# Optimization experiments

Hardware: AMD Instinct MI355X
Metric: run time of the kernel (lower is better)

Reference implementation:

```python
import jax, jax.numpy as jnp
import numpy as np

B, S = 16384, 2048
EPS = 1e-8


def _autocorr(x, lag):
    # Pearson correlation between x[:, :-lag] and x[:, lag:] (ddof cancels).
    a = x[:, :-lag]
    b = x[:, lag:]
    am = a.mean(axis=1, keepdims=True)
    bm = b.mean(axis=1, keepdims=True)
    cov = ((a - am) * (b - bm)).mean(axis=1)
    return cov / (a.std(axis=1) * b.std(axis=1))


def _stat_features(x):
    S_len = x.shape[1]
    mean = x.mean(axis=1)
    xc = x - mean[:, None]
    m2 = (xc ** 2).mean(axis=1)
    m3 = (xc ** 3).mean(axis=1)
    m4 = (xc ** 4).mean(axis=1)
    std = jnp.sqrt(m2)
    min_v = x.min(axis=1)
    max_v = x.max(axis=1)
    q = jnp.percentile(x, jnp.array([25.0, 50.0, 75.0]), axis=1)  # [3, B]
    p25, median, p75 = q[0], q[1], q[2]
    diff = jnp.diff(x, axis=1)
    std_diff = diff.std(axis=1)
    trend = std_diff / (std + EPS)
    ac1 = _autocorr(x, 1)
    ac7 = _autocorr(x, 7)
    ac24 = _autocorr(x, 24)
    cv = std / (jnp.abs(mean) + EPS)
    iqr = p75 - p25
    seasonal = x[:, ::24].var(axis=1) / (m2 + EPS)
    skew = m3 / (m2 ** 1.5)          # scipy.stats.skew, bias=True
    kurt = m4 / (m2 ** 2) - 3.0      # scipy.stats.kurtosis, Fisher, bias=True
    length = jnp.full_like(mean, float(S_len))
    sum_abs_diff = jnp.abs(diff).sum(axis=1)
    mean_abs_diff = jnp.abs(diff).mean(axis=1)
    feats = jnp.stack([mean, std, min_v, max_v, median, trend, ac1, ac7, ac24,
                       cv, iqr, seasonal, skew, kurt, length,
                       sum_abs_diff, mean_abs_diff, std_diff, p25, p75], axis=1)
    return jnp.where(jnp.isfinite(feats), feats, 0.0)


def setup_inputs() -> dict:
    key = jax.random.key(0)
    k0, k1, k2, k3, k4 = jax.random.split(key, 5)
    x = jax.random.normal(k0, (B, S), dtype=jnp.float32)
    W1 = jax.random.normal(k1, (64, 20), dtype=jnp.float32) * 0.1
    b1 = jnp.zeros((64,), dtype=jnp.float32)
    W2 = jax.random.normal(k3, (128, 64), dtype=jnp.float32) * 0.1
    b2 = jnp.zeros((128,), dtype=jnp.float32)
    return {"x": x, "W1": W1, "b1": b1, "W2": W2, "b2": b2}


def reference(x, W1, b1, W2, b2):
    feats = _stat_features(x)                      # [B, 20]
    h = jax.nn.relu(feats @ W1.T + b1)             # [B, 64] (dropout inactive at eval)
    return h @ W2.T + b2                           # [B, 128]
```

## Files before the change

kernel.cpp:

```cpp
#include <hip/hip_runtime.h>
#include <cmath>

constexpr int S_LEN = 2048;
constexpr float EPS = 1e-8f;

typedef unsigned uvec32 __attribute__((ext_vector_type(32)));

__device__ __forceinline__ float fin(float v) { return isfinite(v) ? v : 0.0f; }
__device__ __forceinline__ float rcpf(float x) { return __builtin_amdgcn_rcpf(x); }

__device__ __forceinline__ unsigned f2o_bits(unsigned u) {
    return (u & 0x80000000u) ? ~u : (u | 0x80000000u);
}
__device__ __forceinline__ float o2f(unsigned u) {
    return __uint_as_float((u & 0x80000000u) ? (u ^ 0x80000000u) : ~u);
}

template <int Ctrl, int Rmask>
__device__ __forceinline__ int dpp_zero_i(int x) {
    return __builtin_amdgcn_update_dpp(0, x, Ctrl, Rmask, 0xF, true);
}
template <int Ctrl>
__device__ __forceinline__ int dpp_keep_i(int x) {
    return __builtin_amdgcn_update_dpp(x, x, Ctrl, 0xF, 0xF, false);
}
__device__ __forceinline__ int wred_add_i(int v) {
    v += dpp_zero_i<0xB1, 0xF>(v);
    v += dpp_zero_i<0x4E, 0xF>(v);
    v += dpp_zero_i<0x114, 0xF>(v);
    v += dpp_zero_i<0x118, 0xF>(v);
    v += dpp_zero_i<0x142, 0xA>(v);
    v += dpp_zero_i<0x143, 0xC>(v);
    return __builtin_amdgcn_readlane(v, 63);
}
__device__ __forceinline__ float wred_add_f(float v) {
    #define ADDF(CT, RM) v += __uint_as_float((unsigned)dpp_zero_i<CT, RM>((int)__float_as_uint(v)))
    ADDF(0xB1, 0xF); ADDF(0x4E, 0xF); ADDF(0x114, 0xF);
    ADDF(0x118, 0xF); ADDF(0x142, 0xA); ADDF(0x143, 0xC);
    #undef ADDF
    return __uint_as_float((unsigned)__builtin_amdgcn_readlane((int)__float_as_uint(v), 63));
}
__device__ __forceinline__ float wred_min_f(float v) {
    #define MINF(CT) v = fminf(v, __uint_as_float((unsigned)dpp_keep_i<CT>((int)__float_as_uint(v))))
    MINF(0xB1); MINF(0x4E); MINF(0x114); MINF(0x118); MINF(0x142); MINF(0x143);
    #undef MINF
    return __uint_as_float((unsigned)__builtin_amdgcn_readlane((int)__float_as_uint(v), 63));
}
__device__ __forceinline__ float wred_max_f(float v) {
    #define MAXF(CT) v = fmaxf(v, __uint_as_float((unsigned)dpp_keep_i<CT>((int)__float_as_uint(v))))
    MAXF(0xB1); MAXF(0x4E); MAXF(0x114); MAXF(0x118); MAXF(0x142); MAXF(0x143);
    #undef MAXF
    return __uint_as_float((unsigned)__builtin_amdgcn_readlane((int)__float_as_uint(v), 63));
}
__device__ __forceinline__ unsigned wred_umin(unsigned v) {
    #define MINU(CT) { unsigned t = (unsigned)dpp_keep_i<CT>((int)v); v = v < t ? v : t; }
    MINU(0xB1) MINU(0x4E) MINU(0x114) MINU(0x118) MINU(0x142) MINU(0x143)
    #undef MINU
    return (unsigned)__builtin_amdgcn_readlane((int)v, 63);
}
__device__ __forceinline__ float readlane_f(float x, int l) {
    return __uint_as_float((unsigned)__builtin_amdgcn_readlane((int)__float_as_uint(x), l));
}

__device__ __forceinline__ void transpose32(uvec32& A) {
    #pragma unroll
    for (int k = 0; k < 16; k++) {
        unsigned lo = __builtin_amdgcn_perm(A[k], A[k + 16], 0x07060302u);
        unsigned hi = __builtin_amdgcn_perm(A[k], A[k + 16], 0x05040100u);
        A[k] = lo; A[k + 16] = hi;
    }
    #pragma unroll
    for (int k0 = 0; k0 < 32; k0 += 16) {
        #pragma unroll
        for (int k = k0; k < k0 + 8; k++) {
            unsigned lo = __builtin_amdgcn_perm(A[k], A[k + 8], 0x07030501u);
            unsigned hi = __builtin_amdgcn_perm(A[k], A[k + 8], 0x06020400u);
            A[k] = lo; A[k + 8] = hi;
        }
    }
    #pragma unroll
    for (int j = 4; j; j >>= 1) {
        unsigned m = (j == 4) ? 0x0F0F0F0Fu : (j == 2) ? 0x33333333u : 0x55555555u;
        #pragma unroll
        for (int k = 0; k < 32; k++) {
            if (!(k & j)) {
                unsigned t = (A[k] ^ (A[k | j] >> j)) & m;
                A[k] = A[k] ^ t;
                A[k | j] = A[k | j] ^ (t << j);
            }
        }
    }
}

#define VF(e) __uint_as_float(a[e])

__global__ __launch_bounds__(256) void transpose_w_kernel(
    const float* __restrict__ W1, float* __restrict__ wt)
{
    int tid = blockIdx.x * blockDim.x + threadIdx.x;
    int stride = gridDim.x * blockDim.x;
    for (int n = tid; n < 64 * 20; n += stride) {
        int j = n & 63, k = n >> 6;
        wt[n] = W1[j * 20 + k];
    }
}

__global__ __launch_bounds__(256, 4) void fused_stats_mlp_kernel(
    const float* __restrict__ x, const float* __restrict__ wt,
    const float* __restrict__ b1, const float* __restrict__ W2,
    const float* __restrict__ b2, float* __restrict__ out, int nrows)
{
    __shared__ __align__(16) float sf[4][20];
    __shared__ __align__(16) float hsh[4][64];

    const int gw   = (blockIdx.x * 256 + threadIdx.x) >> 6;
    const int lane = threadIdx.x & 63;
    const int w    = (threadIdx.x >> 6);
    if (gw >= nrows) return;

    uvec32 a;
    const float* xr = x + (size_t)gw * S_LEN + lane * 32;
    #pragma unroll
    for (int q = 0; q < 8; q++) {
        float4 t = reinterpret_cast<const float4*>(xr)[q];
        a[4 * q + 0] = __float_as_uint(t.x); a[4 * q + 1] = __float_as_uint(t.y);
        a[4 * q + 2] = __float_as_uint(t.z); a[4 * q + 3] = __float_as_uint(t.w);
    }

    float s1 = 0.f, s2 = 0.f, sd2 = 0.f, sad = 0.f;
    float p1 = 0.f, p7 = 0.f, p24 = 0.f, se1 = 0.f, se2 = 0.f;
    float mn = VF(0), mx = VF(0);
    #pragma unroll
    for (int e = 0; e < 32; e++) {
        float val = VF(e);
        s1 += val; s2 = fmaf(val, val, s2);
        mn = fminf(mn, val); mx = fmaxf(mx, val);
    }
    #pragma unroll
    for (int e = 0; e < 31; e++) {
        float d = VF(e + 1) - VF(e);
        sd2 = fmaf(d, d, sd2); sad += fabsf(d);
        p1 = fmaf(VF(e), VF(e + 1), p1);
    }
    #pragma unroll
    for (int e = 0; e < 25; e++) p7 = fmaf(VF(e), VF(e + 7), p7);
    #pragma unroll
    for (int e = 0; e < 8; e++)  p24 = fmaf(VF(e), VF(e + 24), p24);

    const bool notlast = (lane < 63);
    #pragma unroll
    for (int j = 0; j < 24; j++) {
        float nb = __shfl_down(VF(j), 1, 64);
        float g = notlast ? nb : 0.f;
        p24 = fmaf(VF(8 + j), g, p24);
        if (j < 7) p7 = fmaf(VF(25 + j), g, p7);
        if (j == 0 && notlast) {
            float d = nb - VF(31);
            sd2 = fmaf(d, d, sd2); sad += fabsf(d);
            p1 = fmaf(VF(31), nb, p1);
        }
    }
    {
        int r3 = lane % 3;
        float sv = (r3 == 0) ? VF(0) : ((r3 == 1) ? VF(16) : VF(8));
        se1 += sv; se2 = fmaf(sv, sv, se2);
        if (r3 == 0) { se1 += VF(24); se2 = fmaf(VF(24), VF(24), se2); }
    }
    float aa = 0, bb = 0, h7v = 0, hq7v = 0;
    #pragma unroll
    for (int e = 0; e < 24; e++) {
        aa += VF(e); bb = fmaf(VF(e), VF(e), bb);
        if (e == 6) { h7v = aa; hq7v = bb; }
    }
    float cc = 0, dd = 0, t7v = 0, tq7v = 0;
    #pragma unroll
    for (int e = 31; e >= 8; e--) {
        cc += VF(e); dd = fmaf(VF(e), VF(e), dd);
        if (e == 25) { t7v = cc; tq7v = dd; }
    }
    const float h1  = readlane_f(VF(0), 0),   t1  = readlane_f(VF(31), 63);
    const float h7  = readlane_f(h7v, 0),     hq7 = readlane_f(hq7v, 0);
    const float h24 = readlane_f(aa, 0),      hq24 = readlane_f(bb, 0);
    const float t7  = readlane_f(t7v, 63),    tq7 = readlane_f(tq7v, 63);
    const float t24 = readlane_f(cc, 63),     tq24 = readlane_f(dd, 63);
    const float hq1 = h1 * h1, tq1 = t1 * t1;

    float S1  = wred_add_f(s1);
    float mean = S1 * (1.0f / S_LEN);
    float S2  = wred_add_f(s2);
    float SD2 = wred_add_f(sd2);
    float SAD = wred_add_f(sad);
    float P1  = wred_add_f(p1);
    float P7  = wred_add_f(p7);
    float P24 = wred_add_f(p24);
    float SE1 = wred_add_f(se1);
    float SE2 = wred_add_f(se2);
    float MN  = wred_min_f(mn);
    float MX  = wred_max_f(mx);

    float c2 = 0.f, c3 = 0.f, c4 = 0.f;
    #pragma unroll
    for (int e = 0; e < 32; e++) {
        float xc = VF(e) - mean;
        float q = xc * xc;
        c2 += q; c3 = fmaf(q, xc, c3); c4 = fmaf(q, q, c4);
    }
    float C2 = wred_add_f(c2), C3 = wred_add_f(c3), C4 = wred_add_f(c4);

    {
        constexpr float invS  = 1.0f / 2048.0f;
        constexpr float invND = 1.0f / 2047.0f;
        const float Sf = (float)S_LEN;
        float m2v = C2 * invS, m3v = C3 * invS, m4v = C4 * invS;
        float stdv = sqrtf(m2v);
        float dmean = (t1 - h1) * invND;
        float dvar = SD2 * invND - dmean * dmean;
        float std_diff = sqrtf(fmaxf(dvar, 0.f));
        float trend = std_diff * rcpf(stdv + EPS);
        float ac[3];
        const float invN[3] = {1.0f / 2047.0f, 1.0f / 2041.0f, 1.0f / 2024.0f};
        const float Ps[3] = {P1, P7, P24};
        const float hd[3] = {h1, h7, h24},   hqv[3] = {hq1, hq7, hq24};
        const float tl[3] = {t1, t7, t24},   tqv[3] = {tq1, tq7, tq24};
        #pragma unroll
        for (int q = 0; q < 3; q++) {
            float in = invN[q];
            float sa = S1 - tl[q], sb = S1 - hd[q];
            float qa = S2 - tqv[q], qb = S2 - hqv[q];
            float am = sa * in, bm = sb * in;
            float cov = Ps[q] * in - am * bm;
            float as_ = sqrtf(fmaxf(qa * in - am * am, 0.f));
            float bs_ = sqrtf(fmaxf(qb * in - bm * bm, 0.f));
            ac[q] = cov * rcpf(as_ * bs_);
        }
        float cv = stdv * rcpf(fabsf(mean) + EPS);
        float sm = SE1 * (1.0f / 86.0f);
        float svar = SE2 * (1.0f / 86.0f) - sm * sm;
        float seasonal = svar * rcpf(m2v + EPS);
        float skew = m3v * rcpf(m2v * stdv);
        float kurt = m4v * rcpf(m2v * m2v) - 3.f;
        if (lane == 0) {
            float* s = sf[w];
            s[0]  = fin(mean);     s[1]  = fin(stdv);
            s[2]  = fin(MN);       s[3]  = fin(MX);
            s[5]  = fin(trend);    s[6]  = fin(ac[0]);
            s[7]  = fin(ac[1]);    s[8]  = fin(ac[2]);
            s[9]  = fin(cv);       s[11] = fin(seasonal);
            s[12] = fin(skew);     s[13] = fin(kurt);
            s[14] = Sf;            s[15] = fin(SAD);
            s[16] = fin(SAD * invND); s[17] = fin(std_diff);
        }
    }

    #pragma unroll
    for (int e = 0; e < 32; e++) a[e] = f2o_bits(a[e]);
    transpose32(a);

    unsigned act0 = ~0u, act1 = ~0u, act2 = ~0u;
    int K0 = 511, K1 = 1023, K2 = 1535;
    int cnt0 = 2048, cnt1 = 2048, cnt2 = 2048;
    unsigned uK0 = 0, uK1 = 0, uK2 = 0;
    #pragma unroll
    for (int b = 31; b >= 0; b--) {
        unsigned mb = a[31 - b];
        unsigned w0 = act0 & mb, w1 = act1 & mb, w2 = act2 & mb;
        int O01 = wred_add_i(__popc(w0) | (__popc(w1) << 16));
        int O2  = wred_add_i(__popc(w2));
        int c0 = cnt0 - (O01 & 0xFFFF);
        int c1 = cnt1 - (int)((unsigned)O01 >> 16);
        int c2i = cnt2 - O2;
        if (K0 < c0)  { act0 ^= w0; cnt0 = c0; }  else { K0 -= c0;  act0 = w0; cnt0 -= c0;  uK0 |= (1u << b); }
        if (K1 < c1)  { act1 ^= w1; cnt1 = c1; }  else { K1 -= c1;  act1 = w1; cnt1 -= c1;  uK1 |= (1u << b); }
        if (K2 < c2i) { act2 ^= w2; cnt2 = c2i; } else { K2 -= c2i; act2 = w2; cnt2 -= c2i; uK2 |= (1u << b); }
    }
    const int eq0 = cnt0, eq1 = cnt1, eq2 = cnt2;

    transpose32(a);
    const unsigned k0p1 = uK0 + 1, k1p1 = uK1 + 1, k2p1 = uK2 + 1;
    unsigned m0 = ~0u, m1 = ~0u, m2 = ~0u;
    #pragma unroll
    for (int e = 0; e < 32; e++) {
        unsigned ue = a[e];
        unsigned d0 = ue - k0p1; m0 = m0 < d0 ? m0 : d0;
        unsigned d1 = ue - k1p1; m1 = m1 < d1 ? m1 : d1;
        unsigned d2 = ue - k2p1; m2 = m2 < d2 ? m2 : d2;
    }
    m0 = wred_umin(m0) + k0p1;
    m1 = wred_umin(m1) + k1p1;
    m2 = wred_umin(m2) + k2p1;

    float v511 = o2f(uK0), v1023 = o2f(uK1), v1535 = o2f(uK2);
    float v512  = (K0 + 1 < eq0) ? v511  : o2f(m0);
    float v1024 = (K1 + 1 < eq1) ? v1023 : o2f(m1);
    float v1536 = (K2 + 1 < eq2) ? v1535 : o2f(m2);
    float p25 = v511 + 0.75f * (v512 - v511);
    float med = 0.5f * (v1023 + v1024);
    float p75 = v1535 + 0.25f * (v1536 - v1535);
    float iqr = p75 - p25;

    if (lane == 0) {
        float* s = sf[w];
        s[4]  = fin(med); s[10] = fin(iqr);
        s[18] = fin(p25); s[19] = fin(p75);
    }
    __asm__ volatile("s_waitcnt lgkmcnt(0)" ::: "memory");
    __builtin_amdgcn_sched_barrier(0);

    const float* W1T = wt;
    const float4* sfv = (const float4*)sf[w];
    float4 f0 = sfv[0], f1 = sfv[1], f2 = sfv[2], f3 = sfv[3], f4 = sfv[4];
    float h = b1[lane];
    h = fmaf(f0.x, W1T[ 0 * 64 + lane], h);
    h = fmaf(f0.y, W1T[ 1 * 64 + lane], h);
    h = fmaf(f0.z, W1T[ 2 * 64 + lane], h);
    h = fmaf(f0.w, W1T[ 3 * 64 + lane], h);
    h = fmaf(f1.x, W1T[ 4 * 64 + lane], h);
    h = fmaf(f1.y, W1T[ 5 * 64 + lane], h);
    h = fmaf(f1.z, W1T[ 6 * 64 + lane], h);
    h = fmaf(f1.w, W1T[ 7 * 64 + lane], h);
    h = fmaf(f2.x, W1T[ 8 * 64 + lane], h);
    h = fmaf(f2.y, W1T[ 9 * 64 + lane], h);
    h = fmaf(f2.z, W1T[10 * 64 + lane], h);
    h = fmaf(f2.w, W1T[11 * 64 + lane], h);
    h = fmaf(f3.x, W1T[12 * 64 + lane], h);
    h = fmaf(f3.y, W1T[13 * 64 + lane], h);
    h = fmaf(f3.z, W1T[14 * 64 + lane], h);
    h = fmaf(f3.w, W1T[15 * 64 + lane], h);
    h = fmaf(f4.x, W1T[16 * 64 + lane], h);
    h = fmaf(f4.y, W1T[17 * 64 + lane], h);
    h = fmaf(f4.z, W1T[18 * 64 + lane], h);
    h = fmaf(f4.w, W1T[19 * 64 + lane], h);
    h = fmaxf(h, 0.f);
    hsh[w][lane] = h;
    __asm__ volatile("s_waitcnt lgkmcnt(0)" ::: "memory");
    __builtin_amdgcn_sched_barrier(0);

    const int j2 = lane * 2;
    float2 b2v = *(const float2*)(b2 + j2);
    float acc0 = b2v.x, acc1 = b2v.y;
    const float4* w2r0 = (const float4*)(W2 + (size_t)j2 * 64);
    const float4* w2r1 = (const float4*)(W2 + (size_t)(j2 + 1) * 64);
    const float4* hv4 = (const float4*)hsh[w];
    #pragma unroll
    for (int q = 0; q < 16; q++) {
        float4 hq = hv4[q];
        float4 wa = w2r0[q];
        float4 wb = w2r1[q];
        acc0 = fmaf(hq.x, wa.x, acc0); acc1 = fmaf(hq.x, wb.x, acc1);
        acc0 = fmaf(hq.y, wa.y, acc0); acc1 = fmaf(hq.y, wb.y, acc1);
        acc0 = fmaf(hq.z, wa.z, acc0); acc1 = fmaf(hq.z, wb.z, acc1);
        acc0 = fmaf(hq.w, wa.w, acc0); acc1 = fmaf(hq.w, wb.w, acc1);
    }
    *(float2*)(out + (size_t)gw * 128 + j2) = make_float2(acc0, acc1);
}

extern "C" void kernel_launch(void* const* d_in, const int* in_sizes, int n_in,
                              void* d_out, int out_size, void* d_ws, size_t ws_size,
                              hipStream_t stream) {
    const float* x  = (const float*)d_in[0];
    const float* W1 = (const float*)d_in[1];
    const float* b1 = (const float*)d_in[2];
    const float* W2 = (const float*)d_in[3];
    const float* b2 = (const float*)d_in[4];
    float* out = (float*)d_out;
    float* wt  = (float*)d_ws;
    int nrows = in_sizes[0] / S_LEN;
    int blocks = (nrows + 3) / 4;
    transpose_w_kernel<<<2, 256, 0, stream>>>(W1, wt);
    fused_stats_mlp_kernel<<<blocks, 256, 0, stream>>>(x, wt, b1, W2, b2, out, nrows);
}
```

Before: 267.7 us.

## Use raw-moment expansion, DPP row shift, branchless radix select, higher occupancy

Central moments m2/m3/m4 now come from raw power sums gathered in the first pass, which removes the second pass over the row and its three extra wave reductions. Several other changes ride along: the lane-neighbour shuffle is replaced by a DPP shift, the head/tail partial sums are merged into one loop selected by lane, the radix-select update becomes branchless selects, the bit-transpose masking is rewritten, and the occupancy hint is raised from 4 to 6 waves. The raw-moment formulas can lose precision through cancellation when the mean is large relative to the spread. The higher occupancy hint may also force register spills given the 32-register row array.

```diff
diff --git a/kernel.cpp b/kernel.cpp
--- a/kernel.cpp
+++ b/kernel.cpp
@@ -23,6 +23,9 @@
 template <int Ctrl>
 __device__ __forceinline__ int dpp_keep_i(int x) {
     return __builtin_amdgcn_update_dpp(x, x, Ctrl, 0xF, 0xF, false);
+}
+__device__ __forceinline__ float dpp_shdn1_f(float x) {
+    return __uint_as_float((unsigned)dpp_zero_i<0x130, 0xF>((int)__float_as_uint(x)));
 }
 __device__ __forceinline__ int wred_add_i(int v) {
     v += dpp_zero_i<0xB1, 0xF>(v);
@@ -80,13 +83,13 @@
     }
     #pragma unroll
     for (int j = 4; j; j >>= 1) {
-        unsigned m = (j == 4) ? 0x0F0F0F0Fu : (j == 2) ? 0x33333333u : 0x55555555u;
+        const unsigned m = (j == 4) ? 0x0F0F0F0Fu : (j == 2) ? 0x33333333u : 0x55555555u;
         #pragma unroll
         for (int k = 0; k < 32; k++) {
             if (!(k & j)) {
-                unsigned t = (A[k] ^ (A[k | j] >> j)) & m;
-                A[k] = A[k] ^ t;
-                A[k | j] = A[k | j] ^ (t << j);
+                unsigned Ak = A[k], Bk = A[k | j];
+                A[k]     = ((Bk >> j) & m) | (Ak & ~m);
+                A[k | j] = ((Ak << j) & ~m) | (Bk & m);
             }
         }
     }
@@ -105,7 +108,7 @@
     }
 }
 
-__global__ __launch_bounds__(256, 4) void fused_stats_mlp_kernel(
+__global__ __launch_bounds__(256, 6) void fused_stats_mlp_kernel(
     const float* __restrict__ x, const float* __restrict__ wt,
     const float* __restrict__ b1, const float* __restrict__ W2,
     const float* __restrict__ b2, float* __restrict__ out, int nrows)
@@ -127,13 +130,15 @@
         a[4 * q + 2] = __float_as_uint(t.z); a[4 * q + 3] = __float_as_uint(t.w);
     }
 
-    float s1 = 0.f, s2 = 0.f, sd2 = 0.f, sad = 0.f;
+    float s1 = 0.f, s2 = 0.f, s3 = 0.f, s4 = 0.f, sd2 = 0.f, sad = 0.f;
     float p1 = 0.f, p7 = 0.f, p24 = 0.f, se1 = 0.f, se2 = 0.f;
     float mn = VF(0), mx = VF(0);
     #pragma unroll
     for (int e = 0; e < 32; e++) {
         float val = VF(e);
-        s1 += val; s2 = fmaf(val, val, s2);
+        float t = val * val;
+        s1 += val; s2 += t;
+        s3 = fmaf(t, val, s3); s4 = fmaf(t, t, s4);
         mn = fminf(mn, val); mx = fmaxf(mx, val);
     }
     #pragma unroll
@@ -150,14 +155,14 @@
     const bool notlast = (lane < 63);
     #pragma unroll
     for (int j = 0; j < 24; j++) {
-        float nb = __shfl_down(VF(j), 1, 64);
-        float g = notlast ? nb : 0.f;
+        float g = dpp_shdn1_f(VF(j));
         p24 = fmaf(VF(8 + j), g, p24);
         if (j < 7) p7 = fmaf(VF(25 + j), g, p7);
-        if (j == 0 && notlast) {
-            float d = nb - VF(31);
-            sd2 = fmaf(d, d, sd2); sad += fabsf(d);
-            p1 = fmaf(VF(31), nb, p1);
+        if (j == 0) {
+            float d = g - VF(31);
+            float dm = notlast ? d : 0.f;
+            sd2 = fmaf(dm, dm, sd2); sad += fabsf(dm);
+            p1 = fmaf(VF(31), g, p1);
         }
     }
     {
@@ -166,28 +171,25 @@
         se1 += sv; se2 = fmaf(sv, sv, se2);
         if (r3 == 0) { se1 += VF(24); se2 = fmaf(VF(24), VF(24), se2); }
     }
-    float aa = 0, bb = 0, h7v = 0, hq7v = 0;
-    #pragma unroll
-    for (int e = 0; e < 24; e++) {
-        aa += VF(e); bb = fmaf(VF(e), VF(e), bb);
-        if (e == 6) { h7v = aa; hq7v = bb; }
-    }
-    float cc = 0, dd = 0, t7v = 0, tq7v = 0;
-    #pragma unroll
-    for (int e = 31; e >= 8; e--) {
-        cc += VF(e); dd = fmaf(VF(e), VF(e), dd);
-        if (e == 25) { t7v = cc; tq7v = dd; }
+    const bool is63 = (lane == 63);
+    float acc1 = 0.f, acc2 = 0.f, ck1 = 0.f, ck2 = 0.f;
+    #pragma unroll
+    for (int i = 0; i < 24; i++) {
+        float pick = is63 ? VF(31 - i) : VF(i);
+        acc1 += pick; acc2 = fmaf(pick, pick, acc2);
+        if (i == 6) { ck1 = acc1; ck2 = acc2; }
     }
     const float h1  = readlane_f(VF(0), 0),   t1  = readlane_f(VF(31), 63);
-    const float h7  = readlane_f(h7v, 0),     hq7 = readlane_f(hq7v, 0);
-    const float h24 = readlane_f(aa, 0),      hq24 = readlane_f(bb, 0);
-    const float t7  = readlane_f(t7v, 63),    tq7 = readlane_f(tq7v, 63);
-    const float t24 = readlane_f(cc, 63),     tq24 = readlane_f(dd, 63);
+    const float h7  = readlane_f(ck1, 0),     hq7 = readlane_f(ck2, 0);
+    const float h24 = readlane_f(acc1, 0),    hq24 = readlane_f(acc2, 0);
+    const float t7  = readlane_f(ck1, 63),    tq7 = readlane_f(ck2, 63);
+    const float t24 = readlane_f(acc1, 63),   tq24 = readlane_f(acc2, 63);
     const float hq1 = h1 * h1, tq1 = t1 * t1;
 
     float S1  = wred_add_f(s1);
-    float mean = S1 * (1.0f / S_LEN);
     float S2  = wred_add_f(s2);
+    float S3  = wred_add_f(s3);
+    float S4  = wred_add_f(s4);
     float SD2 = wred_add_f(sd2);
     float SAD = wred_add_f(sad);
     float P1  = wred_add_f(p1);
@@ -198,20 +200,16 @@
     float MN  = wred_min_f(mn);
     float MX  = wred_max_f(mx);
 
-    float c2 = 0.f, c3 = 0.f, c4 = 0.f;
-    #pragma unroll
-    for (int e = 0; e < 32; e++) {
-        float xc = VF(e) - mean;
-        float q = xc * xc;
-        c2 += q; c3 = fmaf(q, xc, c3); c4 = fmaf(q, q, c4);
-    }
-    float C2 = wred_add_f(c2), C3 = wred_add_f(c3), C4 = wred_add_f(c4);
-
     {
         constexpr float invS  = 1.0f / 2048.0f;
         constexpr float invND = 1.0f / 2047.0f;
         const float Sf = (float)S_LEN;
-        float m2v = C2 * invS, m3v = C3 * invS, m4v = C4 * invS;
+        float mu = S1 * invS;
+        float q2 = S2 * invS, q3 = S3 * invS, q4 = S4 * invS;
+        float mu2 = mu * mu;
+        float m2v = q2 - mu2;
+        float m3v = q3 - 3.f * mu * q2 + 2.f * mu * mu2;
+        float m4v = q4 - 4.f * mu * q3 + 6.f * mu2 * q2 - 3.f * mu2 * mu2;
         float stdv = sqrtf(m2v);
         float dmean = (t1 - h1) * invND;
         float dvar = SD2 * invND - dmean * dmean;
@@ -233,7 +231,7 @@
             float bs_ = sqrtf(fmaxf(qb * in - bm * bm, 0.f));
             ac[q] = cov * rcpf(as_ * bs_);
         }
-        float cv = stdv * rcpf(fabsf(mean) + EPS);
+        float cv = stdv * rcpf(fabsf(mu) + EPS);
         float sm = SE1 * (1.0f / 86.0f);
         float svar = SE2 * (1.0f / 86.0f) - sm * sm;
         float seasonal = svar * rcpf(m2v + EPS);
@@ -241,7 +239,7 @@
         float kurt = m4v * rcpf(m2v * m2v) - 3.f;
         if (lane == 0) {
             float* s = sf[w];
-            s[0]  = fin(mean);     s[1]  = fin(stdv);
+            s[0]  = fin(mu);       s[1]  = fin(stdv);
             s[2]  = fin(MN);       s[3]  = fin(MX);
             s[5]  = fin(trend);    s[6]  = fin(ac[0]);
             s[7]  = fin(ac[1]);    s[8]  = fin(ac[2]);
@@ -269,9 +267,19 @@
         int c0 = cnt0 - (O01 & 0xFFFF);
         int c1 = cnt1 - (int)((unsigned)O01 >> 16);
         int c2i = cnt2 - O2;
-        if (K0 < c0)  { act0 ^= w0; cnt0 = c0; }  else { K0 -= c0;  act0 = w0; cnt0 -= c0;  uK0 |= (1u << b); }
-        if (K1 < c1)  { act1 ^= w1; cnt1 = c1; }  else { K1 -= c1;  act1 = w1; cnt1 -= c1;  uK1 |= (1u << b); }
-        if (K2 < c2i) { act2 ^= w2; cnt2 = c2i; } else { K2 -= c2i; act2 = w2; cnt2 -= c2i; uK2 |= (1u << b); }
+        bool t0 = (K0 >= c0), t1c = (K1 >= c1), t2c = (K2 >= c2i);
+        act0 = t0  ? w0 : (act0 ^ w0);
+        act1 = t1c ? w1 : (act1 ^ w1);
+        act2 = t2c ? w2 : (act2 ^ w2);
+        cnt0 = t0  ? (cnt0 - c0)  : c0;
+        cnt1 = t1c ? (cnt1 - c1)  : c1;
+        cnt2 = t2c ? (cnt2 - c2i) : c2i;
+        K0 = t0  ? (K0 - c0)  : K0;
+        K1 = t1c ? (K1 - c1)  : K1;
+        K2 = t2c ? (K2 - c2i) : K2;
+        uK0 |= t0  ? (1u << b) : 0u;
+        uK1 |= t1c ? (1u << b) : 0u;
+        uK2 |= t2c ? (1u << b) : 0u;
     }
     const int eq0 = cnt0, eq1 = cnt1, eq2 = cnt2;
 
@@ -337,7 +345,7 @@
 
     const int j2 = lane * 2;
     float2 b2v = *(const float2*)(b2 + j2);
-    float acc0 = b2v.x, acc1 = b2v.y;
+    float acc0 = b2v.x, acc1b = b2v.y;
     const float4* w2r0 = (const float4*)(W2 + (size_t)j2 * 64);
     const float4* w2r1 = (const float4*)(W2 + (size_t)(j2 + 1) * 64);
     const float4* hv4 = (const float4*)hsh[w];
@@ -346,12 +354,12 @@
         float4 hq = hv4[q];
         float4 wa = w2r0[q];
         float4 wb = w2r1[q];
-        acc0 = fmaf(hq.x, wa.x, acc0); acc1 = fmaf(hq.x, wb.x, acc1);
-        acc0 = fmaf(hq.y, wa.y, acc0); acc1 = fmaf(hq.y, wb.y, acc1);
-        acc0 = fmaf(hq.z, wa.z, acc0); acc1 = fmaf(hq.z, wb.z, acc1);
-        acc0 = fmaf(hq.w, wa.w, acc0); acc1 = fmaf(hq.w, wb.w, acc1);
-    }
-    *(float2*)(out + (size_t)gw * 128 + j2) = make_float2(acc0, acc1);
+        acc0 = fmaf(hq.x, wa.x, acc0); acc1b = fmaf(hq.x, wb.x, acc1b);
+        acc0 = fmaf(hq.y, wa.y, acc0); acc1b = fmaf(hq.y, wb.y, acc1b);
+        acc0 = fmaf(hq.z, wa.z, acc0); acc1b = fmaf(hq.z, wb.z, acc1b);
+        acc0 = fmaf(hq.w, wa.w, acc0); acc1b = fmaf(hq.w, wb.w, acc1b);
+    }
+    *(float2*)(out + (size_t)gw * 128 + j2) = make_float2(acc0, acc1b);
 }
 
 extern "C" void kernel_launch(void* const* d_in, const int* in_sizes, int n_in,
```

New measurement: 287.1 us. 1.07x slower.
